# Kernel optimization log

Measured on AMD Instinct MI355X. Metric: run time of the kernel, lower is better.

## Reference

```python
import jax, jax.numpy as jnp
import numpy as np

B, NV, NF = 16, 100000, 200000

def _unique_directed_edges(faces):
    # Reproduce the 0/1 dense laplacian: all 6 directed edges per face, deduped.
    f0, f1, f2 = faces[:, 0], faces[:, 1], faces[:, 2]
    e = np.concatenate([
        np.stack([f0, f1], 1), np.stack([f1, f0], 1),
        np.stack([f1, f2], 1), np.stack([f2, f1], 1),
        np.stack([f2, f0], 1), np.stack([f0, f2], 1),
    ], axis=0)
    return np.unique(e, axis=0)  # unique (j,k) pairs == laplacian.bool() entries

def setup_inputs() -> dict:
    key = jax.random.key(0)
    k1, k2 = jax.random.split(key)
    dx = jax.random.normal(k1, (B, NV, 3), dtype=jnp.float32)
    x = jax.random.normal(k2, (B, NV, 3), dtype=jnp.float32)
    rng = np.random.default_rng(0)
    faces = rng.integers(0, NV, size=(NF, 3))
    edges = jnp.asarray(_unique_directed_edges(faces), dtype=jnp.int32)  # [E,2]
    return {"dx": dx, "x": x, "edges": edges}

def reference(dx, x, edges):
    # For every laplacian entry L[j,k]==1 the original computes
    #   diffx[b,j,k]  = sum_i (x[b,k,i]  - x[b,j,i])**2
    #   diffdx[b,j,k] = sum_i (dx[b,k,i] - dx[b,j,i])**2
    # and returns mean_{(j,k) in L} |diffx - diffdx| per batch element.
    j, k = edges[:, 0], edges[:, 1]
    xe = x[:, k] - x[:, j]        # [B,E,3]
    dxe = dx[:, k] - dx[:, j]     # [B,E,3]
    diff = jnp.abs((xe * xe).sum(-1) - (dxe * dxe).sum(-1))  # [B,E]
    return diff.mean(axis=1)      # [B]
```

## Files before the change

kernel.cpp:

```cpp
#include <hip/hip_runtime.h>
#include <math.h>


#define THREADS 256
#define NBLOCKS 2048
#define GROUPS_PER_BLOCK (THREADS / 16)
#define NGROUPS (NBLOCKS * GROUPS_PER_BLOCK)
#define TV 64

__global__ void arap_transpose(const float* __restrict__ x,
                               const float* __restrict__ dx,
                               float* __restrict__ ct,
                               int NV, int B) {
    __shared__ float tile[TV][99];
    int t  = threadIdx.x;
    int v0 = blockIdx.x * TV;
    int bb = t >> 4;
    int vb = t & 15;
    #pragma unroll
    for (int vi = 0; vi < TV / 16; ++vi) {
        int v = v0 + vi * 16 + vb;
        if (v < NV) {
            size_t sx = ((size_t)bb * NV + v) * 3;
            #pragma unroll
            for (int c = 0; c < 3; ++c) {
                tile[vi * 16 + vb][bb * 6 + c]     = x[sx + c];
                tile[vi * 16 + vb][bb * 6 + 3 + c] = dx[sx + c];
            }
        }
    }
    __syncthreads();
    int vg = t >> 4;
    int b2 = t & 15;
    #pragma unroll
    for (int vi = 0; vi < TV / 16; ++vi) {
        int vv = vi * 16 + vg;
        int v  = v0 + vv;
        if (v < NV) {
            float2 a0 = make_float2(tile[vv][b2 * 6 + 0], tile[vv][b2 * 6 + 1]);
            float2 a1 = make_float2(tile[vv][b2 * 6 + 2], tile[vv][b2 * 6 + 3]);
            float2 a2 = make_float2(tile[vv][b2 * 6 + 4], tile[vv][b2 * 6 + 5]);
            float2* dst = (float2*)(ct + ((size_t)v * B + b2) * 6);
            dst[0] = a0; dst[1] = a1; dst[2] = a2;
        }
    }
}

__global__ void arap_main_fused(const float* __restrict__ ct,
                                const int2* __restrict__ edges,
                                float* __restrict__ partial,
                                int E, int chunk) {
    int t   = threadIdx.x;
    int b   = t & 15;
    int sbid = (blockIdx.x & 7) * (NBLOCKS >> 3) + (blockIdx.x >> 3);
    int g    = sbid * GROUPS_PER_BLOCK + (t >> 4);
    long e0 = (long)g * chunk;
    long e1 = e0 + chunk; if (e1 > E) e1 = E;
    const float* base = ct + b * 6;
    float acc = 0.f;
    for (long e = e0; e < e1; ++e) {
        int2 jk = edges[e];
        if (jk.x < jk.y) {
            const float* pj = base + (size_t)jk.x * 96;
            const float* pk = base + (size_t)jk.y * 96;
            float xjx = pj[0], xjy = pj[1], xjz = pj[2];
            float djx = pj[3], djy = pj[4], djz = pj[5];
            float xkx = pk[0], xky = pk[1], xkz = pk[2];
            float dkx = pk[3], dky = pk[4], dkz = pk[5];
            float ex = xkx - xjx, ey = xky - xjy, ez = xkz - xjz;
            float fx = dkx - djx, fy = dky - djy, fz = dkz - djz;
            float sq  = ex * ex + ey * ey + ez * ez;
            float dsq = fx * fx + fy * fy + fz * fz;
            acc += fabsf(sq - dsq);
        }
    }
    acc += __shfl_xor(acc, 16, 64);
    acc += __shfl_xor(acc, 32, 64);
    __shared__ float sacc[THREADS / 64][16];
    int wave = t >> 6, lane = t & 63;
    if (lane < 16) sacc[wave][lane] = acc;
    __syncthreads();
    if (t < 16) {
        float s = 0.f;
        #pragma unroll
        for (int w = 0; w < THREADS / 64; ++w) s += sacc[w][t];
        partial[(size_t)blockIdx.x * 16 + t] = s;
    }
}

__global__ void arap_main_generic(const float* __restrict__ X,
                                  const float* __restrict__ DX,
                                  const int2* __restrict__ edges,
                                  float* __restrict__ partial,
                                  int E, int chunk, int NV) {
    int t = threadIdx.x;
    int b = t & 15;
    int sbid = (blockIdx.x & 7) * (NBLOCKS >> 3) + (blockIdx.x >> 3);
    int g    = sbid * GROUPS_PER_BLOCK + (t >> 4);
    long e0 = (long)g * chunk;
    long e1 = e0 + chunk; if (e1 > E) e1 = E;
    size_t boff = (size_t)b * NV * 3;
    float acc = 0.f;
    for (long e = e0; e < e1; ++e) {
        int2 jk = edges[e];
        if (jk.x < jk.y) {
            size_t aj = boff + (size_t)jk.x * 3, ak = boff + (size_t)jk.y * 3;
            float ex = X[ak] - X[aj], ey = X[ak+1] - X[aj+1], ez = X[ak+2] - X[aj+2];
            float fx = DX[ak] - DX[aj], fy = DX[ak+1] - DX[aj+1], fz = DX[ak+2] - DX[aj+2];
            acc += fabsf((ex*ex + ey*ey + ez*ez) - (fx*fx + fy*fy + fz*fz));
        }
    }
    acc += __shfl_xor(acc, 16, 64);
    acc += __shfl_xor(acc, 32, 64);
    __shared__ float sacc[THREADS / 64][16];
    int wave = t >> 6, lane = t & 63;
    if (lane < 16) sacc[wave][lane] = acc;
    __syncthreads();
    if (t < 16) {
        float s = 0.f;
        #pragma unroll
        for (int w = 0; w < THREADS / 64; ++w) s += sacc[w][t];
        partial[(size_t)blockIdx.x * 16 + t] = s;
    }
}

__global__ void arap_finalize(const float* __restrict__ partial,
                              float* __restrict__ out, int NB, double scale) {
    int b = blockIdx.x;
    int t = threadIdx.x;
    double s = 0.0;
    for (int i = t; i < NB; i += blockDim.x)
        s += (double)partial[(size_t)i * 16 + b];
    #pragma unroll
    for (int off = 32; off; off >>= 1) s += __shfl_xor(s, off, 64);
    __shared__ double ws_[THREADS / 64];
    int wave = t >> 6, lane = t & 63;
    if (lane == 0) ws_[wave] = s;
    __syncthreads();
    if (t == 0) {
        double tot = 0.0;
        #pragma unroll
        for (int w = 0; w < THREADS / 64; ++w) tot += ws_[w];
        out[b] = (float)(tot * scale);
    }
}

extern "C" void kernel_launch(void* const* d_in, const int* in_sizes, int n_in,
                              void* d_out, int out_size, void* d_ws, size_t ws_size,
                              hipStream_t stream) {
    const float* dx    = (const float*)d_in[0];
    const float* x     = (const float*)d_in[1];
    const int*   edges = (const int*)d_in[2];
    float* out = (float*)d_out;

    int B  = out_size;
    int E  = in_sizes[2] / 2;
    int NV = in_sizes[0] / (B * 3);

    int chunk = (E + NGROUPS - 1) / NGROUPS;

    size_t partial_bytes = ((size_t)NBLOCKS * 16 * sizeof(float) + 255) & ~(size_t)255;
    size_t ct_bytes      = (size_t)NV * B * 6 * sizeof(float);

    float* partial = (float*)d_ws;
    double scale = 2.0 / (double)E;

    if (ws_size >= partial_bytes + ct_bytes) {
        float* ct = (float*)((char*)d_ws + partial_bytes);
        arap_transpose<<<(NV + TV - 1) / TV, THREADS, 0, stream>>>(x, dx, ct, NV, B);
        arap_main_fused<<<NBLOCKS, THREADS, 0, stream>>>(ct, (const int2*)edges,
                                                         partial, E, chunk);
    } else {
        arap_main_generic<<<NBLOCKS, THREADS, 0, stream>>>(x, dx, (const int2*)edges,
                                                           partial, E, chunk, NV);
    }
    arap_finalize<<<B, THREADS, 0, stream>>>(partial, out, NBLOCKS, scale);
}
```

Baseline: 166.9 us.

## Compact valid edges per wave via ballot and unroll gathers for more memory parallelism

The fused kernel now gives each wave a fixed tile of 128 edges. It loads them as int4 pairs, keeps only the j<k edges using ballot/popcount into LDS, and spreads the compacted list over four 16-lane subgroups. Each subgroup then gathers up to four edges per iteration as float2 loads. This is meant to remove the branch divergence and serial per-group chunk loop, and to expose more independent loads in flight. In exchange it adds LDS staging, a barrier, and a grid size that depends on E.

```diff
diff --git a/kernel.cpp b/kernel.cpp
--- a/kernel.cpp
+++ b/kernel.cpp
@@ -3,10 +3,10 @@
 
 
 #define THREADS 256
-#define NBLOCKS 2048
-#define GROUPS_PER_BLOCK (THREADS / 16)
-#define NGROUPS (NBLOCKS * GROUPS_PER_BLOCK)
 #define TV 64
+#define WEDGES 128
+#define BEDGES (WEDGES * 4)
+#define GENBLOCKS 2048
 
 __global__ void arap_transpose(const float* __restrict__ x,
                                const float* __restrict__ dx,
@@ -46,44 +46,86 @@
     }
 }
 
+#define LOAD6(v, A0, A1, A2) { \
+    const float2* _p = (const float2*)(vbase + (size_t)(v) * 96); \
+    A0 = _p[0]; A1 = _p[1]; A2 = _p[2]; }
+
+#define EV(J0, J1, J2, K0, K1, K2) ({ \
+    float _ex = K0.x - J0.x, _ey = K0.y - J0.y, _ez = K1.x - J1.x; \
+    float _fx = K1.y - J1.y, _fy = K2.x - J2.x, _fz = K2.y - J2.y; \
+    fabsf((_ex*_ex + _ey*_ey + _ez*_ez) - (_fx*_fx + _fy*_fy + _fz*_fz)); })
+
 __global__ void arap_main_fused(const float* __restrict__ ct,
                                 const int2* __restrict__ edges,
                                 float* __restrict__ partial,
-                                int E, int chunk) {
-    int t   = threadIdx.x;
-    int b   = t & 15;
-    int sbid = (blockIdx.x & 7) * (NBLOCKS >> 3) + (blockIdx.x >> 3);
-    int g    = sbid * GROUPS_PER_BLOCK + (t >> 4);
-    long e0 = (long)g * chunk;
-    long e1 = e0 + chunk; if (e1 > E) e1 = E;
-    const float* base = ct + b * 6;
+                                long E, int grid8) {
+    int t    = threadIdx.x;
+    int lane = t & 63;
+    int wv   = t >> 6;
+    int b    = t & 15;
+    int sg   = (t >> 4) & 3;
+
+    __shared__ int2  cbuf[4][WEDGES];
+    __shared__ float sacc[4][16];
+
+    int sbid = (blockIdx.x & 7) * (grid8 >> 3) + (blockIdx.x >> 3);
+    long base_e = ((long)sbid * 4 + wv) * WEDGES;
+
+    long eidx = base_e + 2 * lane;
+    int4 q = make_int4(0, 0, 0, 0);
+    if (eidx + 1 < E)      q = *(const int4*)(&edges[eidx]);
+    else if (eidx < E)   { int2 e2 = edges[eidx]; q.x = e2.x; q.y = e2.y; }
+    bool p0 = q.x < q.y;
+    bool p1 = q.z < q.w;
+    unsigned long long m0 = __ballot(p0);
+    unsigned long long m1 = __ballot(p1);
+    unsigned long long pre = ((unsigned long long)1 << lane) - 1;
+    int n0    = __popcll(m0);
+    int npass = n0 + __popcll(m1);
+    if (p0) cbuf[wv][__popcll(m0 & pre)]      = make_int2(q.x, q.y);
+    if (p1) cbuf[wv][n0 + __popcll(m1 & pre)] = make_int2(q.z, q.w);
+    __syncthreads();
+
+    const float* vbase = ct + b * 6;
     float acc = 0.f;
-    for (long e = e0; e < e1; ++e) {
-        int2 jk = edges[e];
-        if (jk.x < jk.y) {
-            const float* pj = base + (size_t)jk.x * 96;
-            const float* pk = base + (size_t)jk.y * 96;
-            float xjx = pj[0], xjy = pj[1], xjz = pj[2];
-            float djx = pj[3], djy = pj[4], djz = pj[5];
-            float xkx = pk[0], xky = pk[1], xkz = pk[2];
-            float dkx = pk[3], dky = pk[4], dkz = pk[5];
-            float ex = xkx - xjx, ey = xky - xjy, ez = xkz - xjz;
-            float fx = dkx - djx, fy = dky - djy, fz = dkz - djz;
-            float sq  = ex * ex + ey * ey + ez * ez;
-            float dsq = fx * fx + fy * fy + fz * fz;
-            acc += fabsf(sq - dsq);
-        }
-    }
+    int i = sg;
+    for (; i + 12 < npass; i += 16) {
+        int2 E0 = cbuf[wv][i], E1 = cbuf[wv][i + 4];
+        int2 E2 = cbuf[wv][i + 8], E3 = cbuf[wv][i + 12];
+        float2 a0,a1,a2, b0,b1,b2, c0,c1,c2, d0,d1,d2;
+        float2 e0,e1,e2, f0,f1,f2, g0,g1,g2, h0,h1,h2;
+        LOAD6(E0.x, a0,a1,a2)  LOAD6(E0.y, b0,b1,b2)
+        LOAD6(E1.x, c0,c1,c2)  LOAD6(E1.y, d0,d1,d2)
+        LOAD6(E2.x, e0,e1,e2)  LOAD6(E2.y, f0,f1,f2)
+        LOAD6(E3.x, g0,g1,g2)  LOAD6(E3.y, h0,h1,h2)
+        float v0 = EV(a0,a1,a2, b0,b1,b2);
+        float v1 = EV(c0,c1,c2, d0,d1,d2);
+        float v2 = EV(e0,e1,e2, f0,f1,f2);
+        float v3 = EV(g0,g1,g2, h0,h1,h2);
+        acc += (v0 + v1) + (v2 + v3);
+    }
+    for (; i + 4 < npass; i += 8) {
+        int2 E0 = cbuf[wv][i], E1 = cbuf[wv][i + 4];
+        float2 a0,a1,a2, b0,b1,b2, c0,c1,c2, d0,d1,d2;
+        LOAD6(E0.x, a0,a1,a2)  LOAD6(E0.y, b0,b1,b2)
+        LOAD6(E1.x, c0,c1,c2)  LOAD6(E1.y, d0,d1,d2)
+        acc += EV(a0,a1,a2, b0,b1,b2) + EV(c0,c1,c2, d0,d1,d2);
+    }
+    for (; i < npass; i += 4) {
+        int2 E0 = cbuf[wv][i];
+        float2 a0,a1,a2, b0,b1,b2;
+        LOAD6(E0.x, a0,a1,a2)  LOAD6(E0.y, b0,b1,b2)
+        acc += EV(a0,a1,a2, b0,b1,b2);
+    }
+
     acc += __shfl_xor(acc, 16, 64);
     acc += __shfl_xor(acc, 32, 64);
-    __shared__ float sacc[THREADS / 64][16];
-    int wave = t >> 6, lane = t & 63;
-    if (lane < 16) sacc[wave][lane] = acc;
+    if (lane < 16) sacc[wv][lane] = acc;
     __syncthreads();
     if (t < 16) {
         float s = 0.f;
         #pragma unroll
-        for (int w = 0; w < THREADS / 64; ++w) s += sacc[w][t];
+        for (int w = 0; w < 4; ++w) s += sacc[w][t];
         partial[(size_t)blockIdx.x * 16 + t] = s;
     }
 }
@@ -92,22 +134,23 @@
                                   const float* __restrict__ DX,
                                   const int2* __restrict__ edges,
                                   float* __restrict__ partial,
-                                  int E, int chunk, int NV) {
+                                  long E, int chunk, int NV, int B) {
     int t = threadIdx.x;
     int b = t & 15;
-    int sbid = (blockIdx.x & 7) * (NBLOCKS >> 3) + (blockIdx.x >> 3);
-    int g    = sbid * GROUPS_PER_BLOCK + (t >> 4);
+    int g = blockIdx.x * (THREADS / 16) + (t >> 4);
     long e0 = (long)g * chunk;
     long e1 = e0 + chunk; if (e1 > E) e1 = E;
     size_t boff = (size_t)b * NV * 3;
     float acc = 0.f;
-    for (long e = e0; e < e1; ++e) {
-        int2 jk = edges[e];
-        if (jk.x < jk.y) {
-            size_t aj = boff + (size_t)jk.x * 3, ak = boff + (size_t)jk.y * 3;
-            float ex = X[ak] - X[aj], ey = X[ak+1] - X[aj+1], ez = X[ak+2] - X[aj+2];
-            float fx = DX[ak] - DX[aj], fy = DX[ak+1] - DX[aj+1], fz = DX[ak+2] - DX[aj+2];
-            acc += fabsf((ex*ex + ey*ey + ez*ez) - (fx*fx + fy*fy + fz*fz));
+    if (b < B) {
+        for (long e = e0; e < e1; ++e) {
+            int2 jk = edges[e];
+            if (jk.x < jk.y) {
+                size_t aj = boff + (size_t)jk.x * 3, ak = boff + (size_t)jk.y * 3;
+                float ex = X[ak] - X[aj], ey = X[ak+1] - X[aj+1], ez = X[ak+2] - X[aj+2];
+                float fx = DX[ak] - DX[aj], fy = DX[ak+1] - DX[aj+1], fz = DX[ak+2] - DX[aj+2];
+                acc += fabsf((ex*ex + ey*ey + ez*ez) - (fx*fx + fy*fy + fz*fz));
+            }
         }
     }
     acc += __shfl_xor(acc, 16, 64);
@@ -153,26 +196,30 @@
     const int*   edges = (const int*)d_in[2];
     float* out = (float*)d_out;
 
-    int B  = out_size;
-    int E  = in_sizes[2] / 2;
-    int NV = in_sizes[0] / (B * 3);
-
-    int chunk = (E + NGROUPS - 1) / NGROUPS;
-
-    size_t partial_bytes = ((size_t)NBLOCKS * 16 * sizeof(float) + 255) & ~(size_t)255;
+    int B   = out_size;
+    long E  = in_sizes[2] / 2;
+    int NV  = in_sizes[0] / (B * 3);
+
+    int gridE = (int)((E + BEDGES - 1) / BEDGES);
+    int grid8 = ((gridE + 7) / 8) * 8;
+
+    size_t partial_bytes = ((size_t)grid8 * 16 * sizeof(float) + 255) & ~(size_t)255;
     size_t ct_bytes      = (size_t)NV * B * 6 * sizeof(float);
 
     float* partial = (float*)d_ws;
     double scale = 2.0 / (double)E;
 
-    if (ws_size >= partial_bytes + ct_bytes) {
+    if (B == 16 && ws_size >= partial_bytes + ct_bytes) {
         float* ct = (float*)((char*)d_ws + partial_bytes);
         arap_transpose<<<(NV + TV - 1) / TV, THREADS, 0, stream>>>(x, dx, ct, NV, B);
-        arap_main_fused<<<NBLOCKS, THREADS, 0, stream>>>(ct, (const int2*)edges,
-                                                         partial, E, chunk);
+        arap_main_fused<<<grid8, THREADS, 0, stream>>>(ct, (const int2*)edges,
+                                                       partial, E, grid8);
+        arap_finalize<<<B, THREADS, 0, stream>>>(partial, out, grid8, scale);
     } else {
-        arap_main_generic<<<NBLOCKS, THREADS, 0, stream>>>(x, dx, (const int2*)edges,
-                                                           partial, E, chunk, NV);
-    }
-    arap_finalize<<<B, THREADS, 0, stream>>>(partial, out, NBLOCKS, scale);
-}
+        int ggrid = GENBLOCKS;
+        int chunk = (int)((E + (long)ggrid * 16 - 1) / ((long)ggrid * 16));
+        arap_main_generic<<<ggrid, THREADS, 0, stream>>>(x, dx, (const int2*)edges,
+                                                         partial, E, chunk, NV, B);
+        arap_finalize<<<B, THREADS, 0, stream>>>(partial, out, ggrid, scale);
+    }
+}
```

After: 155.4 us. 6.9% less time.

## Compact j<k edges per wave in LDS and batch vertex gathers

Applied to the files above, without the earlier changes.

The main kernel now gives each wave a contiguous edge range. Each wave loads edges in chunks of 256 with vectorized int4 loads and compacts the edges with j<k into shared memory using ballot/popcount, so no lanes sit idle on the skipped half of the edges. The gather loop then processes four edges per step with float2 loads, two batches in flight, to raise memory-level parallelism. The transpose kernel is rewritten to emit coalesced float4 stores of whole 96-float vertex rows. The cost is higher register pressure and padding work, plus a specialization to B==16 for the fast path.

```diff
diff --git a/kernel.cpp b/kernel.cpp
--- a/kernel.cpp
+++ b/kernel.cpp
@@ -3,87 +3,137 @@
 
 
 #define THREADS 256
-#define NBLOCKS 2048
-#define GROUPS_PER_BLOCK (THREADS / 16)
-#define NGROUPS (NBLOCKS * GROUPS_PER_BLOCK)
-#define TV 64
-
-__global__ void arap_transpose(const float* __restrict__ x,
-                               const float* __restrict__ dx,
-                               float* __restrict__ ct,
-                               int NV, int B) {
-    __shared__ float tile[TV][99];
+#define MAIN_BLOCKS 1024
+#define NWAVES (MAIN_BLOCKS * 4)
+#define CHUNK 256
+#define TTV 32
+
+__global__ __launch_bounds__(256) void arap_transpose(
+        const float* __restrict__ x, const float* __restrict__ dx,
+        float* __restrict__ ct, int NV) {
+    __shared__ float tile[TTV * 100];
     int t  = threadIdx.x;
-    int v0 = blockIdx.x * TV;
-    int bb = t >> 4;
-    int vb = t & 15;
+    int v0 = blockIdx.x * TTV;
+    int bb = t >> 4, vb = t & 15;
     #pragma unroll
-    for (int vi = 0; vi < TV / 16; ++vi) {
-        int v = v0 + vi * 16 + vb;
+    for (int vi = 0; vi < 2; ++vi) {
+        int vloc = vi * 16 + vb;
+        int v = v0 + vloc;
         if (v < NV) {
-            size_t sx = ((size_t)bb * NV + v) * 3;
-            #pragma unroll
-            for (int c = 0; c < 3; ++c) {
-                tile[vi * 16 + vb][bb * 6 + c]     = x[sx + c];
-                tile[vi * 16 + vb][bb * 6 + 3 + c] = dx[sx + c];
+            const float* px  = x  + ((size_t)bb * NV + v) * 3;
+            const float* pdx = dx + ((size_t)bb * NV + v) * 3;
+            float a0 = px[0],  a1 = px[1],  a2 = px[2];
+            float b0 = pdx[0], b1 = pdx[1], b2 = pdx[2];
+            float* tr = tile + vloc * 100 + bb * 6;
+            tr[0] = a0; tr[1] = a1; tr[2] = a2;
+            tr[3] = b0; tr[4] = b1; tr[5] = b2;
+        }
+    }
+    __syncthreads();
+    if (v0 + TTV <= NV) {
+        float4* outv = (float4*)(ct + (size_t)v0 * 96);
+        #pragma unroll
+        for (int i = 0; i < 3; ++i) {
+            int f = t * 3 + i;
+            int o = f * 4;
+            int v = o / 96, r = o - v * 96;
+            const float* ts = tile + v * 100 + r;
+            outv[f] = make_float4(ts[0], ts[1], ts[2], ts[3]);
+        }
+    } else {
+        #pragma unroll
+        for (int i = 0; i < 3; ++i) {
+            int f = t * 3 + i, o = f * 4;
+            int v = o / 96, r = o - v * 96;
+            if (v0 + v < NV) {
+                float* dst = ct + (size_t)(v0 + v) * 96 + r;
+                const float* ts = tile + v * 100 + r;
+                dst[0] = ts[0]; dst[1] = ts[1]; dst[2] = ts[2]; dst[3] = ts[3];
             }
         }
     }
-    __syncthreads();
-    int vg = t >> 4;
-    int b2 = t & 15;
-    #pragma unroll
-    for (int vi = 0; vi < TV / 16; ++vi) {
-        int vv = vi * 16 + vg;
-        int v  = v0 + vv;
-        if (v < NV) {
-            float2 a0 = make_float2(tile[vv][b2 * 6 + 0], tile[vv][b2 * 6 + 1]);
-            float2 a1 = make_float2(tile[vv][b2 * 6 + 2], tile[vv][b2 * 6 + 3]);
-            float2 a2 = make_float2(tile[vv][b2 * 6 + 4], tile[vv][b2 * 6 + 5]);
-            float2* dst = (float2*)(ct + ((size_t)v * B + b2) * 6);
-            dst[0] = a0; dst[1] = a1; dst[2] = a2;
-        }
-    }
-}
-
-__global__ void arap_main_fused(const float* __restrict__ ct,
-                                const int2* __restrict__ edges,
-                                float* __restrict__ partial,
-                                int E, int chunk) {
-    int t   = threadIdx.x;
-    int b   = t & 15;
-    int sbid = (blockIdx.x & 7) * (NBLOCKS >> 3) + (blockIdx.x >> 3);
-    int g    = sbid * GROUPS_PER_BLOCK + (t >> 4);
-    long e0 = (long)g * chunk;
-    long e1 = e0 + chunk; if (e1 > E) e1 = E;
-    const float* base = ct + b * 6;
+}
+
+#define RP(v) ((const float2*)(vbase + (size_t)(v) * 96))
+#define LOAD4(R, S) { \
+    int2 Ea = cbuf[wv][S], Eb = cbuf[wv][(S)+1], Ec = cbuf[wv][(S)+2], Ed = cbuf[wv][(S)+3]; \
+    const float2 *ja=RP(Ea.x),*ka=RP(Ea.y),*jb=RP(Eb.x),*kb=RP(Eb.y); \
+    const float2 *jc=RP(Ec.x),*kc=RP(Ec.y),*jd=RP(Ed.x),*kd=RP(Ed.y); \
+    R[0]=ja[0];  R[1]=ja[1];  R[2]=ja[2];  R[3]=ka[0];  R[4]=ka[1];  R[5]=ka[2]; \
+    R[6]=jb[0];  R[7]=jb[1];  R[8]=jb[2];  R[9]=kb[0];  R[10]=kb[1]; R[11]=kb[2]; \
+    R[12]=jc[0]; R[13]=jc[1]; R[14]=jc[2]; R[15]=kc[0]; R[16]=kc[1]; R[17]=kc[2]; \
+    R[18]=jd[0]; R[19]=jd[1]; R[20]=jd[2]; R[21]=kd[0]; R[22]=kd[1]; R[23]=kd[2]; }
+#define EV1(J0,J1,J2,K0,K1,K2) ({ \
+    float _ex=K0.x-J0.x, _ey=K0.y-J0.y, _ez=K1.x-J1.x; \
+    float _fx=K1.y-J1.y, _fy=K2.x-J2.x, _fz=K2.y-J2.y; \
+    fabsf((_ex*_ex+_ey*_ey+_ez*_ez)-(_fx*_fx+_fy*_fy+_fz*_fz)); })
+#define COMP4(R) ((EV1(R[0],R[1],R[2],R[3],R[4],R[5]) + EV1(R[6],R[7],R[8],R[9],R[10],R[11])) + \
+                  (EV1(R[12],R[13],R[14],R[15],R[16],R[17]) + EV1(R[18],R[19],R[20],R[21],R[22],R[23])))
+
+__global__ __launch_bounds__(256, 4) void arap_main_fused(
+        const float* __restrict__ ct, const int2* __restrict__ edges,
+        float* __restrict__ partial, long E, long spw) {
+    __shared__ int2  cbuf[4][CHUNK + 16];
+    __shared__ float sacc[4][16];
+    int t = threadIdx.x, lane = t & 63, wv = t >> 6, b = t & 15, sg = (t >> 4) & 3;
+    int sbid = (blockIdx.x & 7) * (MAIN_BLOCKS / 8) + (blockIdx.x >> 3);
+    long wid = (long)sbid * 4 + wv;
+    long e0 = wid * spw;
+    long e1 = e0 + spw; if (e1 > E) e1 = E;
+    const float* vbase = ct + b * 6;
     float acc = 0.f;
-    for (long e = e0; e < e1; ++e) {
-        int2 jk = edges[e];
-        if (jk.x < jk.y) {
-            const float* pj = base + (size_t)jk.x * 96;
-            const float* pk = base + (size_t)jk.y * 96;
-            float xjx = pj[0], xjy = pj[1], xjz = pj[2];
-            float djx = pj[3], djy = pj[4], djz = pj[5];
-            float xkx = pk[0], xky = pk[1], xkz = pk[2];
-            float dkx = pk[3], dky = pk[4], dkz = pk[5];
-            float ex = xkx - xjx, ey = xky - xjy, ez = xkz - xjz;
-            float fx = dkx - djx, fy = dky - djy, fz = dkz - djz;
-            float sq  = ex * ex + ey * ey + ez * ez;
-            float dsq = fx * fx + fy * fy + fz * fz;
-            acc += fabsf(sq - dsq);
-        }
-    }
+
+    for (long cbase = e0; cbase < e1; cbase += CHUNK) {
+        int cnt = (int)((e1 - cbase < CHUNK) ? (e1 - cbase) : CHUNK);
+        long eidx = cbase + 4 * lane;
+        int base4 = 4 * lane;
+        int4 qa = make_int4(0,0,0,0), qb = make_int4(0,0,0,0);
+        if (base4 + 3 < cnt) {
+            qa = *(const int4*)(&edges[eidx]);
+            qb = *(const int4*)(&edges[eidx + 2]);
+        } else if (base4 < cnt) {
+            int2 t0 = edges[eidx];
+            int2 t1 = (base4+1 < cnt) ? edges[eidx+1] : make_int2(0,0);
+            int2 t2 = (base4+2 < cnt) ? edges[eidx+2] : make_int2(0,0);
+            qa = make_int4(t0.x, t0.y, t1.x, t1.y);
+            qb = make_int4(t2.x, t2.y, 0, 0);
+        }
+        bool p0 = (base4+0 < cnt) && (qa.x < qa.y);
+        bool p1 = (base4+1 < cnt) && (qa.z < qa.w);
+        bool p2 = (base4+2 < cnt) && (qb.x < qb.y);
+        bool p3 = (base4+3 < cnt) && (qb.z < qb.w);
+        unsigned long long m0 = __ballot(p0), m1 = __ballot(p1);
+        unsigned long long m2 = __ballot(p2), m3 = __ballot(p3);
+        unsigned long long pre = ((unsigned long long)1 << lane) - 1;
+        int c0 = __popcll(m0), c1 = c0 + __popcll(m1), c2 = c1 + __popcll(m2);
+        int npass = c2 + __popcll(m3);
+        if (p0) cbuf[wv][     __popcll(m0 & pre)] = make_int2(qa.x, qa.y);
+        if (p1) cbuf[wv][c0 + __popcll(m1 & pre)] = make_int2(qa.z, qa.w);
+        if (p2) cbuf[wv][c1 + __popcll(m2 & pre)] = make_int2(qb.x, qb.y);
+        if (p3) cbuf[wv][c2 + __popcll(m3 & pre)] = make_int2(qb.z, qb.w);
+        int npad = (npass + 15) & ~15;
+        if (lane < npad - npass) cbuf[wv][npass + lane] = make_int2(0, 0);
+
+        int npg  = npad >> 2;
+        int gbeg = sg * npg, gend = gbeg + npg;
+        float2 A[24], Bst[24];
+        for (int s = gbeg; s < gend; s += 8) {
+            LOAD4(A, s);
+            bool hasB = (s + 4 < gend);
+            if (hasB) LOAD4(Bst, s + 4);
+            acc += COMP4(A);
+            if (hasB) acc += COMP4(Bst);
+        }
+    }
+
     acc += __shfl_xor(acc, 16, 64);
     acc += __shfl_xor(acc, 32, 64);
-    __shared__ float sacc[THREADS / 64][16];
-    int wave = t >> 6, lane = t & 63;
-    if (lane < 16) sacc[wave][lane] = acc;
+    if (lane < 16) sacc[wv][lane] = acc;
     __syncthreads();
     if (t < 16) {
         float s = 0.f;
         #pragma unroll
-        for (int w = 0; w < THREADS / 64; ++w) s += sacc[w][t];
+        for (int w = 0; w < 4; ++w) s += sacc[w][t];
         partial[(size_t)blockIdx.x * 16 + t] = s;
     }
 }
@@ -92,22 +142,23 @@
                                   const float* __restrict__ DX,
                                   const int2* __restrict__ edges,
                                   float* __restrict__ partial,
-                                  int E, int chunk, int NV) {
+                                  long E, int chunk, int NV, int B) {
     int t = threadIdx.x;
     int b = t & 15;
-    int sbid = (blockIdx.x & 7) * (NBLOCKS >> 3) + (blockIdx.x >> 3);
-    int g    = sbid * GROUPS_PER_BLOCK + (t >> 4);
+    int g = blockIdx.x * (THREADS / 16) + (t >> 4);
     long e0 = (long)g * chunk;
     long e1 = e0 + chunk; if (e1 > E) e1 = E;
     size_t boff = (size_t)b * NV * 3;
     float acc = 0.f;
-    for (long e = e0; e < e1; ++e) {
-        int2 jk = edges[e];
-        if (jk.x < jk.y) {
-            size_t aj = boff + (size_t)jk.x * 3, ak = boff + (size_t)jk.y * 3;
-            float ex = X[ak] - X[aj], ey = X[ak+1] - X[aj+1], ez = X[ak+2] - X[aj+2];
-            float fx = DX[ak] - DX[aj], fy = DX[ak+1] - DX[aj+1], fz = DX[ak+2] - DX[aj+2];
-            acc += fabsf((ex*ex + ey*ey + ez*ez) - (fx*fx + fy*fy + fz*fz));
+    if (b < B) {
+        for (long e = e0; e < e1; ++e) {
+            int2 jk = edges[e];
+            if (jk.x < jk.y) {
+                size_t aj = boff + (size_t)jk.x * 3, ak = boff + (size_t)jk.y * 3;
+                float ex = X[ak] - X[aj], ey = X[ak+1] - X[aj+1], ez = X[ak+2] - X[aj+2];
+                float fx = DX[ak] - DX[aj], fy = DX[ak+1] - DX[aj+1], fz = DX[ak+2] - DX[aj+2];
+                acc += fabsf((ex*ex + ey*ey + ez*ez) - (fx*fx + fy*fy + fz*fz));
+            }
         }
     }
     acc += __shfl_xor(acc, 16, 64);
@@ -153,26 +204,30 @@
     const int*   edges = (const int*)d_in[2];
     float* out = (float*)d_out;
 
-    int B  = out_size;
-    int E  = in_sizes[2] / 2;
-    int NV = in_sizes[0] / (B * 3);
-
-    int chunk = (E + NGROUPS - 1) / NGROUPS;
-
-    size_t partial_bytes = ((size_t)NBLOCKS * 16 * sizeof(float) + 255) & ~(size_t)255;
-    size_t ct_bytes      = (size_t)NV * B * 6 * sizeof(float);
+    int B   = out_size;
+    long E  = in_sizes[2] / 2;
+    int NV  = in_sizes[0] / (B * 3);
+
+    long spw = (E + NWAVES - 1) / NWAVES;
+    spw = (spw + 3) & ~(long)3;
+
+    size_t partial_bytes = ((size_t)MAIN_BLOCKS * 16 * sizeof(float) + 255) & ~(size_t)255;
+    size_t ct_bytes      = (size_t)NV * 16 * 6 * sizeof(float);
 
     float* partial = (float*)d_ws;
     double scale = 2.0 / (double)E;
 
-    if (ws_size >= partial_bytes + ct_bytes) {
+    if (B == 16 && ws_size >= partial_bytes + ct_bytes) {
         float* ct = (float*)((char*)d_ws + partial_bytes);
-        arap_transpose<<<(NV + TV - 1) / TV, THREADS, 0, stream>>>(x, dx, ct, NV, B);
-        arap_main_fused<<<NBLOCKS, THREADS, 0, stream>>>(ct, (const int2*)edges,
-                                                         partial, E, chunk);
+        arap_transpose<<<(NV + TTV - 1) / TTV, THREADS, 0, stream>>>(x, dx, ct, NV);
+        arap_main_fused<<<MAIN_BLOCKS, THREADS, 0, stream>>>(ct, (const int2*)edges,
+                                                             partial, E, spw);
+        arap_finalize<<<B, THREADS, 0, stream>>>(partial, out, MAIN_BLOCKS, scale);
     } else {
-        arap_main_generic<<<NBLOCKS, THREADS, 0, stream>>>(x, dx, (const int2*)edges,
-                                                           partial, E, chunk, NV);
-    }
-    arap_finalize<<<B, THREADS, 0, stream>>>(partial, out, NBLOCKS, scale);
-}
+        int ggrid = 2048;
+        int chunk = (int)((E + (long)ggrid * 16 - 1) / ((long)ggrid * 16));
+        arap_main_generic<<<ggrid, THREADS, 0, stream>>>(x, dx, (const int2*)edges,
+                                                         partial, E, chunk, NV, B);
+        arap_finalize<<<B, THREADS, 0, stream>>>(partial, out, ggrid, scale);
+    }
+}
```

Measured after the change: 156.0 us. 1.07x faster.
